# Kernel tuning notes

Measured on AMD Instinct MI355X. Metric: run time of the kernel, lower is better.

The kernel has to match this reference:

```python
import jax, jax.numpy as jnp
import numpy as np

N, CIN, T, HF, WF = 1, 64, 8, 96, 96
C = 256
H, W = HF // 4, WF // 4
K = 27  # 3 dilations (1,3,5) x 3x3 kernel taps

# kernel-tap offsets, ordered: dilation-major, then row-major 3x3 (matches cat order)
_OFFS = np.array([(oy * d, ox * d) for d in (1, 3, 5) for oy in (-1, 0, 1) for ox in (-1, 0, 1)], dtype=np.float32)


def setup_inputs() -> dict:
    key = jax.random.key(0)
    ks = jax.random.split(key, 6)
    return {
        "input": jax.random.normal(ks[0], (N, CIN, T, HF, WF), jnp.float32),
        "flow": 2.0 * jax.random.normal(ks[1], (N, 2, T, H, W), jnp.float32),
        "w_node": 0.02 * jax.random.normal(ks[2], (C, CIN, 4, 4), jnp.float32),  # Conv3d(64,256,(1,4,4)) with unit time-kernel squeezed
        "b_node": jnp.zeros((C,), jnp.float32),
        "w_up": 0.02 * jax.random.normal(ks[3], (C, 64, 4, 4), jnp.float32),  # ConvTranspose3d(256,64,(1,4,4)) weight [in,out,kh,kw]
        "b_up": jnp.zeros((64,), jnp.float32),
        "w_out": 0.05 * jax.random.normal(ks[4], (64, 64), jnp.float32),  # 1x1x1 Conv3d(64,64)
        "b_out": jnp.zeros((64,), jnp.float32),
        "B": T,
    }


def _deform_sample(node, flow):
    # Deformable neighbor sampling for all 3 dilations at once.
    # node [N,C,T,H,W], flow [N,2,T,H,W] (y,x offsets) -> neighbour [N,C,T,H,W,K]
    n, c, t, h, w = node.shape
    off = jnp.asarray(_OFFS)  # [K,2]
    yy = jnp.arange(h, dtype=node.dtype)[:, None]   # [H,1]
    xx = jnp.arange(w, dtype=node.dtype)[None, :]   # [1,W]
    # sampling positions [N,T,K,H,W]
    py = (yy + off[:, 0][:, None, None]) + flow[:, 0][:, :, None]
    px = (xx + off[:, 1][:, None, None]) + flow[:, 1][:, :, None]
    y0 = jnp.floor(py)
    x0 = jnp.floor(px)
    ty = py - y0
    tx = px - x0
    y0 = y0.astype(jnp.int32)
    x0 = x0.astype(jnp.int32)
    nf = node.transpose(0, 2, 1, 3, 4).reshape(n, t, c, h * w)  # [N,T,C,HW]

    def gather(yi, xi):
        valid = ((yi >= 0) & (yi < h) & (xi >= 0) & (xi < w)).astype(node.dtype)
        idx = jnp.clip(yi, 0, h - 1) * w + jnp.clip(xi, 0, w - 1)  # [N,T,K,H,W]
        idx = jnp.broadcast_to(idx.reshape(n, t, 1, K * h * w), (n, t, c, K * h * w))
        v = jnp.take_along_axis(nf, idx, axis=-1).reshape(n, t, c, K, h, w)
        return v * valid[:, :, None]  # zero-pad outside

    samp = (gather(y0, x0) * ((1 - ty) * (1 - tx))[:, :, None]
            + gather(y0, x0 + 1) * ((1 - ty) * tx)[:, :, None]
            + gather(y0 + 1, x0) * (ty * (1 - tx))[:, :, None]
            + gather(y0 + 1, x0 + 1) * (ty * tx)[:, :, None])  # [N,T,C,K,H,W]
    return samp.transpose(0, 2, 1, 4, 5, 3)  # [N,C,T,H,W,K]


def reference(input, flow, w_node, b_node, w_up, b_up, w_out, b_out, B):
    n, cin, t, hf, wf = input.shape
    h, w = hf // 4, wf // 4
    # layer_node: kernel==stride (1,4,4) conv == non-overlapping 4x4 patch projection
    xr = input.reshape(n, cin, t, h, 4, w, 4)
    node = jnp.einsum('ncthawb,ocab->nothw', xr, w_node) + b_node[None, :, None, None, None]  # [N,C,T,H,W]
    c = node.shape[1]

    neighbour = _deform_sample(node, flow)  # [N,C,T,H,W,27] == cat(dcn1,dcn2,dcn3)

    nhw = n * h * w
    node_b = node.transpose(0, 3, 4, 2, 1).reshape(nhw, t, c)                      # [NHW,B,C]
    nb_a = neighbour.transpose(0, 3, 4, 1, 2, 5).reshape(nhw, c, t * K)            # [NHW,C,B*27]
    A = node_b @ nb_a                                                              # [NHW,B,B*27]
    nb_b = neighbour.transpose(0, 3, 4, 2, 5, 1).reshape(nhw, t * K, c)            # [NHW,B*27,C]
    out = (1.0 / 216.0) * (A @ nb_b)                                               # [NHW,B,C]
    out = out.reshape(n, h, w, t, c).transpose(0, 4, 3, 1, 2)                      # [N,C,T,H,W]

    # layer_out: ConvTranspose (k==stride, pad 0) == per-pixel 4x4 block expansion, then 1x1x1 conv
    up = jnp.einsum('ncthw,coab->nothawb', out, w_up).reshape(n, 64, t, 4 * h, 4 * w)
    up = up + b_up[None, :, None, None, None]
    return jnp.einsum('ncthw,oc->nothw', up, w_out) + b_out[None, :, None, None, None]
```

## Files before the change

### kernel.cpp

```cpp
#include <hip/hip_runtime.h>


typedef unsigned short ushort_t;
typedef ushort_t ushort8 __attribute__((ext_vector_type(8)));
typedef __bf16 bf16x8 __attribute__((ext_vector_type(8)));
typedef __bf16 bf16x2 __attribute__((ext_vector_type(2)));
typedef float f32x4 __attribute__((ext_vector_type(4)));
typedef unsigned int uint4v __attribute__((ext_vector_type(4)));

#define NSTR 264
#define TSTR 34
#define ASTR 40

#define OFF_NH0   0
#define OFF_NH1   16896
#define OFF_NT0   33792
#define OFF_NT1   51200
#define OFF_AS    68608
#define OFF_BASES 69888
#define OFF_WTS   73472
#define ATTN_LDS  77056

__device__ __forceinline__ ushort_t f2bf(float f) {
    __bf16 h = (__bf16)f;
    return __builtin_bit_cast(ushort_t, h);
}
__device__ __forceinline__ float blo(unsigned u) { return __uint_as_float(u << 16); }
__device__ __forceinline__ float bhi(unsigned u) { return __uint_as_float(u & 0xffff0000u); }
__device__ __forceinline__ unsigned pk2(float a, float b) {
    bf16x2 v = { (__bf16)a, (__bf16)b };
    return __builtin_bit_cast(unsigned, v);
}
__device__ __forceinline__ unsigned pk2h(__bf16 a, __bf16 b) {
    bf16x2 v = { a, b };
    return __builtin_bit_cast(unsigned, v);
}
__device__ __forceinline__ void gld_lds16(const void* g, void* l) {
    __builtin_amdgcn_global_load_lds(
        (const __attribute__((address_space(1))) unsigned*)g,
        (__attribute__((address_space(3))) unsigned*)l, 16, 0, 0);
}

__global__ __launch_bounds__(256) void k_prep(
    const float* __restrict__ w_node, const float* __restrict__ w_up,
    const float* __restrict__ w_out, const float* __restrict__ b_up,
    const float* __restrict__ b_out,
    ushort_t* __restrict__ w_node_perm, ushort_t* __restrict__ Wf_perm,
    float* __restrict__ bias_tot)
{
    __shared__ float wout_s[4096];
    int tid = threadIdx.x;
    for (int i = tid; i < 4096; i += 256) wout_s[i] = w_out[i];
    __syncthreads();
    int gid = blockIdx.x * 256 + tid;
    #pragma unroll
    for (int r = 0; r < 4; ++r) {
        int e = gid + r * 65536;
        {
            int k = e & 1023, n = e >> 10;
            w_node_perm[(((k >> 3) << 8) + n) * 8 + (k & 7)] = f2bf(w_node[n * 1024 + k]);
        }
        {
            int n = e & 1023, k = e >> 10;
            int o = n >> 4, ab = n & 15;
            const float* wo = wout_s + o * 64;
            const float* wu = w_up + (k << 10) + ab;
            float s = 0.f;
            #pragma unroll 8
            for (int c = 0; c < 64; ++c) s += wo[c] * wu[c << 4];
            Wf_perm[(((k >> 3) << 10) + n) * 8 + (k & 7)] = f2bf(s);
        }
    }
    if (blockIdx.x == 0 && tid < 64) {
        float s = b_out[tid];
        const float* wo = wout_s + tid * 64;
        #pragma unroll 8
        for (int c = 0; c < 64; ++c) s += wo[c] * b_up[c];
        bias_tot[tid] = s;
    }
}

template<int FINAL>
__global__ __launch_bounds__(256) void k_gemm(
    const float* __restrict__ input, const ushort_t* __restrict__ a_bf,
    const ushort_t* __restrict__ w_perm, const float* __restrict__ bias,
    ushort_t* __restrict__ node_bf, float* __restrict__ dout)
{
    constexpr int KS = FINAL ? 4 : 16;
    constexpr int N  = FINAL ? 1024 : 256;
    constexpr int BN = FINAL ? 128 : 64;
    constexpr int NI = FINAL ? 2 : 1;
    constexpr int RB = BN / 32;
    __shared__ __align__(16) ushort_t A_lds[2][2048];
    __shared__ __align__(16) ushort_t B_lds[2][BN * 64];
    int tid  = threadIdx.x;
    int lane = tid & 63, wid = tid >> 6;
    int g = lane >> 4, r16 = lane & 15;
    int m0 = blockIdx.x * 32, n0 = blockIdx.y * BN;

    const float*   inpA = nullptr;
    const ushort_t* finA = nullptr;
    int ldsA_slot;
    if constexpr (!FINAL) {
        int mA = tid & 31, kcA = tid >> 5;
        int m = m0 + mA;
        int t = m / 576, hw = m % 576, hh = hw / 24, ww = hw % 24;
        inpA = input + (size_t)(kcA >> 1) * 73728 + t * 9216 + hh * 384 + ww * 4 + (kcA & 1) * 192;
        ldsA_slot = (kcA * 32 + mA) * 8;
    } else {
        int m = m0 + (tid >> 3), q = tid & 7;
        finA = a_bf + m * 256 + ((q ^ (m & 7)) * 8);
        ldsA_slot = tid * 8;
    }

    f32x4 acc[2][NI];
    #pragma unroll
    for (int i = 0; i < 2; ++i)
        #pragma unroll
        for (int j = 0; j < NI; ++j) acc[i][j] = (f32x4){0.f, 0.f, 0.f, 0.f};

    float4 fa, fb;
    #pragma unroll
    for (int r = 0; r < RB; ++r) {
        int s = r * 256 + tid;
        int kc = s / BN, n = s % BN;
        gld_lds16(w_perm + (size_t)((kc * N + n0 + n) * 8), &B_lds[0][s * 8]);
    }
    if constexpr (FINAL) {
        gld_lds16(finA, &A_lds[0][ldsA_slot]);
    } else {
        fa = *(const float4*)(inpA);
        fb = *(const float4*)(inpA + 96);
        uint4v p;
        p.x = pk2(fa.x, fa.y); p.y = pk2(fa.z, fa.w);
        p.z = pk2(fb.x, fb.y); p.w = pk2(fb.z, fb.w);
        *(uint4v*)&A_lds[0][ldsA_slot] = p;
    }
    __syncthreads();

    for (int kb = 0; kb < KS; ++kb) {
        int cur = kb & 1, nxt = cur ^ 1;
        bool more = (kb + 1 < KS);
        if (more) {
            #pragma unroll
            for (int r = 0; r < RB; ++r) {
                int s = r * 256 + tid;
                int kc = s / BN, n = s % BN;
                gld_lds16(w_perm + (size_t)((((kb + 1) * 8 + kc) * N + n0 + n) * 8),
                          &B_lds[nxt][s * 8]);
            }
            if constexpr (FINAL) {
                gld_lds16(finA + (kb + 1) * 64, &A_lds[nxt][ldsA_slot]);
            } else {
                fa = *(const float4*)(inpA + (size_t)(kb + 1) * 294912);
                fb = *(const float4*)(inpA + (size_t)(kb + 1) * 294912 + 96);
            }
        }
        bf16x8 af[2][2], bfr[NI][2];
        #pragma unroll
        for (int mi = 0; mi < 2; ++mi)
            #pragma unroll
            for (int ks = 0; ks < 2; ++ks) {
                int idx;
                if constexpr (!FINAL) idx = ((ks * 4 + g) * 32 + mi * 16 + r16) * 8;
                else                  idx = (mi * 16 + r16) * 64 + (((ks * 4 + g) ^ (r16 & 7)) * 8);
                af[mi][ks] = __builtin_bit_cast(bf16x8, *(const ushort8*)&A_lds[cur][idx]);
            }
        #pragma unroll
        for (int ni = 0; ni < NI; ++ni)
            #pragma unroll
            for (int ks = 0; ks < 2; ++ks) {
                int idx = ((ks * 4 + g) * BN + wid * (BN / 4) + ni * 16 + r16) * 8;
                bfr[ni][ks] = __builtin_bit_cast(bf16x8, *(const ushort8*)&B_lds[cur][idx]);
            }
        #pragma unroll
        for (int mi = 0; mi < 2; ++mi)
            #pragma unroll
            for (int ni = 0; ni < NI; ++ni)
                #pragma unroll
                for (int ks = 0; ks < 2; ++ks)
                    acc[mi][ni] = __builtin_amdgcn_mfma_f32_16x16x32_bf16(
                        af[mi][ks], bfr[ni][ks], acc[mi][ni], 0, 0, 0);
        if constexpr (!FINAL) {
            if (more) {
                uint4v p;
                p.x = pk2(fa.x, fa.y); p.y = pk2(fa.z, fa.w);
                p.z = pk2(fb.x, fb.y); p.w = pk2(fb.z, fb.w);
                *(uint4v*)&A_lds[nxt][ldsA_slot] = p;
            }
        }
        __syncthreads();
    }

    if constexpr (!FINAL) {
        int n = n0 + wid * 16 + r16;
        float bv = bias[n];
        #pragma unroll
        for (int mi = 0; mi < 2; ++mi)
            #pragma unroll
            for (int rr = 0; rr < 4; ++rr) {
                int m = m0 + mi * 16 + 4 * g + rr;
                node_bf[(size_t)m * 256 + n] = f2bf(acc[mi][0][rr] + bv);
            }
    } else {
        #pragma unroll
        for (int ni = 0; ni < NI; ++ni) {
            int n = n0 + wid * 32 + ni * 16 + r16;
            int o = n >> 4, aa = (n >> 2) & 3, bb = n & 3;
            float bv = bias[o];
            #pragma unroll
            for (int mi = 0; mi < 2; ++mi)
                #pragma unroll
                for (int rr = 0; rr < 4; ++rr) {
                    int m = m0 + mi * 16 + 4 * g + rr;
                    int t = m / 576, hw = m % 576, hh = hw / 24, ww = hw % 24;
                    dout[((size_t)(o * 8 + t) * 96 + hh * 4 + aa) * 96 + ww * 4 + bb]
                        = acc[mi][ni][rr] + bv;
                }
        }
    }
}

__device__ __forceinline__ void combine8(
    uint4v t0, uint4v t1, uint4v t2, uint4v t3,
    uint4v t4, uint4v t5, uint4v t6, uint4v t7,
    float4 wA, float4 wB, ushort_t* __restrict__ nh, ushort_t* __restrict__ nt,
    int jl, int c0)
{
    uint4v outA, outB;
    #pragma unroll
    for (int p = 0; p < 4; ++p) {
        unsigned a0 = t0[p], a1 = t1[p], a2 = t2[p], a3 = t3[p];
        unsigned b0 = t4[p], b1 = t5[p], b2 = t6[p], b3 = t7[p];
        float aL = wA.x * blo(a0) + wA.y * blo(a1) + wA.z * blo(a2) + wA.w * blo(a3);
        float aH = wA.x * bhi(a0) + wA.y * bhi(a1) + wA.z * bhi(a2) + wA.w * bhi(a3);
        float bL = wB.x * blo(b0) + wB.y * blo(b1) + wB.z * blo(b2) + wB.w * blo(b3);
        float bH = wB.x * bhi(b0) + wB.y * bhi(b1) + wB.z * bhi(b2) + wB.w * bhi(b3);
        __bf16 cAL = (__bf16)aL, cAH = (__bf16)aH;
        __bf16 cBL = (__bf16)bL, cBH = (__bf16)bH;
        outA[p] = pk2h(cAL, cAH);
        outB[p] = pk2h(cBL, cBH);
        *(unsigned*)(nt + (c0 + 2 * p) * TSTR + jl)     = pk2h(cAL, cBL);
        *(unsigned*)(nt + (c0 + 2 * p + 1) * TSTR + jl) = pk2h(cAH, cBH);
    }
    *(uint4v*)(nh + jl * NSTR + c0)       = outA;
    *(uint4v*)(nh + (jl + 1) * NSTR + c0) = outB;
}

__global__ __launch_bounds__(256) void k_attn(
    const ushort_t* __restrict__ node_bf, const float* __restrict__ flow,
    ushort_t* __restrict__ out_bf)
{
    extern __shared__ char smem[];
    ushort_t* A_s   = (ushort_t*)(smem + OFF_AS);
    int*      bases = (int*)(smem + OFF_BASES);
    float*    wts   = (float*)(smem + OFF_WTS);

    int tid  = threadIdx.x;
    int pos  = blockIdx.x;
    int h    = pos / 24, w = pos % 24;
    int lane = tid & 63, wid = tid >> 6;
    int g    = lane >> 4, r16 = lane & 15;

    if (tid < 224) {
        int j = tid;
        float w00 = 0, w01 = 0, w10 = 0, w11 = 0;
        int b00 = 0, b01 = 0, b10 = 0, b11 = 0;
        if (j < 216) {
            int tt = j / 27, kk = j - tt * 27;
            int d  = 2 * (kk / 9) + 1;
            int oy = (kk / 3) % 3 - 1, ox = kk % 3 - 1;
            float fy = flow[tt * 576 + pos];
            float fx = flow[4608 + tt * 576 + pos];
            float py = (float)(h + oy * d) + fy;
            float px = (float)(w + ox * d) + fx;
            float fy0 = floorf(py), fx0 = floorf(px);
            int y0 = (int)fy0, x0 = (int)fx0;
            float ty = py - fy0, tx = px - fx0;
            int y0c = min(max(y0, 0), 23), y1c = min(max(y0 + 1, 0), 23);
            int x0c = min(max(x0, 0), 23), x1c = min(max(x0 + 1, 0), 23);
            float vy0 = (y0 >= 0 && y0 < 24) ? 1.f : 0.f;
            float vy1 = (y0 >= -1 && y0 < 23) ? 1.f : 0.f;
            float vx0 = (x0 >= 0 && x0 < 24) ? 1.f : 0.f;
            float vx1 = (x0 >= -1 && x0 < 23) ? 1.f : 0.f;
            w00 = (1.f - ty) * (1.f - tx) * vy0 * vx0;
            w01 = (1.f - ty) * tx * vy0 * vx1;
            w10 = ty * (1.f - tx) * vy1 * vx0;
            w11 = ty * tx * vy1 * vx1;
            int base_t = tt * 576 * 256;
            b00 = base_t + (y0c * 24 + x0c) * 256;
            b01 = base_t + (y0c * 24 + x1c) * 256;
            b10 = base_t + (y1c * 24 + x0c) * 256;
            b11 = base_t + (y1c * 24 + x1c) * 256;
        }
        bases[j * 4 + 0] = b00; bases[j * 4 + 1] = b01;
        bases[j * 4 + 2] = b10; bases[j * 4 + 3] = b11;
        wts[j * 4 + 0] = w00; wts[j * 4 + 1] = w01;
        wts[j * 4 + 2] = w10; wts[j * 4 + 3] = w11;
    }
    for (int i = tid; i < 320; i += 256) ((unsigned*)A_s)[i] = 0;

    bf16x8 nbf[8];
    if (wid < 2) {
        int t = r16;
        const ushort_t* src = node_bf + ((size_t)(t & 7) * 576 + pos) * 256 + g * 8;
        ushort8 uz = {};
        #pragma unroll
        for (int s = 0; s < 8; ++s) {
            ushort8 uu = *(const ushort8*)(src + s * 32);
            nbf[s] = __builtin_bit_cast(bf16x8, (t < 8) ? uu : uz);
        }
    }

    f32x4 oacc[4];
    #pragma unroll
    for (int i = 0; i < 4; ++i) oacc[i] = (f32x4){0.f, 0.f, 0.f, 0.f};

    __syncthreads();

    const int jp2  = (tid >> 4) * 2;
    const int c0lo = (tid & 15) * 16;
    const int c0hi = c0lo + 8;

    uint4v rA0, rA1, rA2, rA3, rA4, rA5, rA6, rA7;
    uint4v rB0, rB1, rB2, rB3, rB4, rB5, rB6, rB7;

    #define PREFETCH(TILE) do {                                   \
        int jA_ = (TILE) * 32 + jp2;                              \
        int4 bsA_ = *(const int4*)&bases[jA_ * 4];                \
        int4 bsB_ = *(const int4*)&bases[jA_ * 4 + 4];            \
        rA0 = *(const uint4v*)(node_bf + bsA_.x + c0lo);          \
        rA1 = *(const uint4v*)(node_bf + bsA_.y + c0lo);          \
        rA2 = *(const uint4v*)(node_bf + bsA_.z + c0lo);          \
        rA3 = *(const uint4v*)(node_bf + bsA_.w + c0lo);          \
        rA4 = *(const uint4v*)(node_bf + bsB_.x + c0lo);          \
        rA5 = *(const uint4v*)(node_bf + bsB_.y + c0lo);          \
        rA6 = *(const uint4v*)(node_bf + bsB_.z + c0lo);          \
        rA7 = *(const uint4v*)(node_bf + bsB_.w + c0lo);          \
        rB0 = *(const uint4v*)(node_bf + bsA_.x + c0hi);          \
        rB1 = *(const uint4v*)(node_bf + bsA_.y + c0hi);          \
        rB2 = *(const uint4v*)(node_bf + bsA_.z + c0hi);          \
        rB3 = *(const uint4v*)(node_bf + bsA_.w + c0hi);          \
        rB4 = *(const uint4v*)(node_bf + bsB_.x + c0hi);          \
        rB5 = *(const uint4v*)(node_bf + bsB_.y + c0hi);          \
        rB6 = *(const uint4v*)(node_bf + bsB_.z + c0hi);          \
        rB7 = *(const uint4v*)(node_bf + bsB_.w + c0hi);          \
    } while (0)

    #define COMBINE(TILE, nh, nt) do {                                          \
        int jC_ = (TILE) * 32 + jp2;                                            \
        float4 wA_ = *(const float4*)&wts[jC_ * 4];                             \
        float4 wB_ = *(const float4*)&wts[jC_ * 4 + 4];                         \
        combine8(rA0, rA1, rA2, rA3, rA4, rA5, rA6, rA7, wA_, wB_, nh, nt, jp2, c0lo); \
        combine8(rB0, rB1, rB2, rB3, rB4, rB5, rB6, rB7, wA_, wB_, nh, nt, jp2, c0hi); \
    } while (0)

    PREFETCH(0);
    COMBINE(0, (ushort_t*)(smem + OFF_NH0), (ushort_t*)(smem + OFF_NT0));
    PREFETCH(1);
    __syncthreads();

    for (int k = 0; k < 7; ++k) {
        int cur = k & 1;
        ushort_t* nh = (ushort_t*)(smem + (cur ? OFF_NH1 : OFF_NH0));
        ushort_t* nt = (ushort_t*)(smem + (cur ? OFF_NT1 : OFF_NT0));

        if (wid < 2) {
            f32x4 aacc = {0.f, 0.f, 0.f, 0.f};
            int jbase = wid * 16;
            #pragma unroll
            for (int s = 0; s < 8; ++s) {
                const ushort_t* bp = nh + (jbase + r16) * NSTR + s * 32 + g * 8;
                bf16x8 bfrag = __builtin_bit_cast(bf16x8, *(const ushort8*)bp);
                aacc = __builtin_amdgcn_mfma_f32_16x16x32_bf16(nbf[s], bfrag, aacc, 0, 0, 0);
            }
            if (g < 2) {
                #pragma unroll
                for (int rr = 0; rr < 4; ++rr)
                    A_s[(4 * g + rr) * ASTR + jbase + r16] = f2bf(aacc[rr] * (1.f / 216.f));
            }
        }
        __syncthreads();

        {
            bf16x8 afrag = __builtin_bit_cast(bf16x8, *(const ushort8*)(A_s + r16 * ASTR + g * 8));
            #pragma unroll
            for (int i = 0; i < 4; ++i) {
                const ushort_t* tp = nt + (wid * 64 + i * 16 + r16) * TSTR + g * 8;
                uint4v uv;
                uv.x = *(const unsigned*)(tp);
                uv.y = *(const unsigned*)(tp + 2);
                uv.z = *(const unsigned*)(tp + 4);
                uv.w = *(const unsigned*)(tp + 6);
                bf16x8 bfrag = __builtin_bit_cast(bf16x8, uv);
                oacc[i] = __builtin_amdgcn_mfma_f32_16x16x32_bf16(afrag, bfrag, oacc[i], 0, 0, 0);
            }
        }
        if (k < 6) {
            ushort_t* nh2 = (ushort_t*)(smem + (cur ? OFF_NH0 : OFF_NH1));
            ushort_t* nt2 = (ushort_t*)(smem + (cur ? OFF_NT0 : OFF_NT1));
            COMBINE(k + 1, nh2, nt2);
            if (k <= 4) PREFETCH(k + 2);
        }
        __syncthreads();
    }
    #undef PREFETCH
    #undef COMBINE

    if (g < 2) {
        #pragma unroll
        for (int i = 0; i < 4; ++i) {
            int c = wid * 64 + i * 16 + r16;
            #pragma unroll
            for (int rr = 0; rr < 4; ++rr) {
                int t = 4 * g + rr;
                out_bf[((size_t)t * 576 + pos) * 256 + c] = f2bf(oacc[i][rr]);
            }
        }
    }
}

extern "C" void kernel_launch(void* const* d_in, const int* in_sizes, int n_in,
                              void* d_out, int out_size, void* d_ws, size_t ws_size,
                              hipStream_t stream) {
    (void)in_sizes; (void)n_in; (void)out_size; (void)ws_size;
    const float* input  = (const float*)d_in[0];
    const float* flow   = (const float*)d_in[1];
    const float* w_node = (const float*)d_in[2];
    const float* b_node = (const float*)d_in[3];
    const float* w_up   = (const float*)d_in[4];
    const float* b_up   = (const float*)d_in[5];
    const float* w_out  = (const float*)d_in[6];
    const float* b_out  = (const float*)d_in[7];
    float* dout = (float*)d_out;

    char* wsb = (char*)d_ws;
    ushort_t* node_bf = (ushort_t*)wsb;
    ushort_t* out_bf  = (ushort_t*)(wsb + 2359296);
    ushort_t* w_np    = (ushort_t*)(wsb + 4718592);
    ushort_t* wf_p    = (ushort_t*)(wsb + 5242880);
    float*    bias_t  = (float*)(wsb + 5767168);

    k_prep<<<256, 256, 0, stream>>>(w_node, w_up, w_out, b_up, b_out, w_np, wf_p, bias_t);
    k_gemm<0><<<dim3(144, 4), 256, 0, stream>>>(input, nullptr, w_np, b_node, node_bf, nullptr);
    hipFuncSetAttribute(reinterpret_cast<const void*>(k_attn),
                        hipFuncAttributeMaxDynamicSharedMemorySize, ATTN_LDS);
    k_attn<<<576, 256, ATTN_LDS, stream>>>(node_bf, flow, out_bf);
    k_gemm<1><<<dim3(144, 8), 256, 0, stream>>>(nullptr, out_bf, wf_p, bias_t, nullptr, dout);
}
```

Baseline: 74.62 us.

## Drop transposed neighbour LDS copy, stage final GEMM epilogue through LDS

The attention kernel no longer writes a second, transposed copy of the sampled neighbour tile into LDS. The second MFMA now builds its B fragments with eight strided 16-bit LDS reads from the row-major tile, which roughly halves LDS use per block and may allow more blocks per CU, at the cost of more LDS read instructions. The final GEMM epilogue now stages accumulators in LDS so each thread can write a float4 to the output instead of scattered scalar stores. The weight-prep reduction also gets four independent accumulators to shorten its dependency chain.

```diff
diff --git a/kernel.cpp b/kernel.cpp
--- a/kernel.cpp
+++ b/kernel.cpp
@@ -9,17 +9,14 @@
 typedef unsigned int uint4v __attribute__((ext_vector_type(4)));
 
 #define NSTR 264
-#define TSTR 34
 #define ASTR 40
 
 #define OFF_NH0   0
 #define OFF_NH1   16896
-#define OFF_NT0   33792
-#define OFF_NT1   51200
-#define OFF_AS    68608
-#define OFF_BASES 69888
-#define OFF_WTS   73472
-#define ATTN_LDS  77056
+#define OFF_AS    33792
+#define OFF_BASES 35072
+#define OFF_WTS   38656
+#define ATTN_LDS  42240
 
 __device__ __forceinline__ ushort_t f2bf(float f) {
     __bf16 h = (__bf16)f;
@@ -29,10 +26,6 @@
 __device__ __forceinline__ float bhi(unsigned u) { return __uint_as_float(u & 0xffff0000u); }
 __device__ __forceinline__ unsigned pk2(float a, float b) {
     bf16x2 v = { (__bf16)a, (__bf16)b };
-    return __builtin_bit_cast(unsigned, v);
-}
-__device__ __forceinline__ unsigned pk2h(__bf16 a, __bf16 b) {
-    bf16x2 v = { a, b };
     return __builtin_bit_cast(unsigned, v);
 }
 __device__ __forceinline__ void gld_lds16(const void* g, void* l) {
@@ -65,10 +58,15 @@
             int o = n >> 4, ab = n & 15;
             const float* wo = wout_s + o * 64;
             const float* wu = w_up + (k << 10) + ab;
-            float s = 0.f;
-            #pragma unroll 8
-            for (int c = 0; c < 64; ++c) s += wo[c] * wu[c << 4];
-            Wf_perm[(((k >> 3) << 10) + n) * 8 + (k & 7)] = f2bf(s);
+            float s0 = 0.f, s1 = 0.f, s2 = 0.f, s3 = 0.f;
+            #pragma unroll 4
+            for (int c = 0; c < 64; c += 4) {
+                s0 += wo[c]     * wu[c << 4];
+                s1 += wo[c + 1] * wu[(c + 1) << 4];
+                s2 += wo[c + 2] * wu[(c + 2) << 4];
+                s3 += wo[c + 3] * wu[(c + 3) << 4];
+            }
+            Wf_perm[(((k >> 3) << 10) + n) * 8 + (k & 7)] = f2bf((s0 + s1) + (s2 + s3));
         }
     }
     if (blockIdx.x == 0 && tid < 64) {
@@ -203,20 +201,30 @@
                 node_bf[(size_t)m * 256 + n] = f2bf(acc[mi][0][rr] + bv);
             }
     } else {
+        constexpr int EPS = 132;
+        float* ep = (float*)&B_lds[0][0];
         #pragma unroll
         for (int ni = 0; ni < NI; ++ni) {
-            int n = n0 + wid * 32 + ni * 16 + r16;
-            int o = n >> 4, aa = (n >> 2) & 3, bb = n & 3;
-            float bv = bias[o];
+            int n = wid * 32 + ni * 16 + r16;
             #pragma unroll
             for (int mi = 0; mi < 2; ++mi)
                 #pragma unroll
-                for (int rr = 0; rr < 4; ++rr) {
-                    int m = m0 + mi * 16 + 4 * g + rr;
-                    int t = m / 576, hw = m % 576, hh = hw / 24, ww = hw % 24;
-                    dout[((size_t)(o * 8 + t) * 96 + hh * 4 + aa) * 96 + ww * 4 + bb]
-                        = acc[mi][ni][rr] + bv;
-                }
+                for (int rr = 0; rr < 4; ++rr)
+                    ep[(mi * 16 + 4 * g + rr) * EPS + n] = acc[mi][ni][rr];
+        }
+        __syncthreads();
+        #pragma unroll
+        for (int r = 0; r < 4; ++r) {
+            int task = r * 256 + tid;
+            int mloc = task & 31, nb4 = task >> 5;
+            float4 v = *(const float4*)&ep[mloc * EPS + nb4 * 4];
+            int n = n0 + nb4 * 4;
+            int o = n >> 4, aa = (n >> 2) & 3;
+            float bv = bias[o];
+            int m = m0 + mloc;
+            int t = m / 576, hw = m % 576, hh = hw / 24, ww = hw % 24;
+            float* dst = dout + ((size_t)(o * 8 + t) * 96 + hh * 4 + aa) * 96 + ww * 4;
+            *(float4*)dst = make_float4(v.x + bv, v.y + bv, v.z + bv, v.w + bv);
         }
     }
 }
@@ -224,8 +232,7 @@
 __device__ __forceinline__ void combine8(
     uint4v t0, uint4v t1, uint4v t2, uint4v t3,
     uint4v t4, uint4v t5, uint4v t6, uint4v t7,
-    float4 wA, float4 wB, ushort_t* __restrict__ nh, ushort_t* __restrict__ nt,
-    int jl, int c0)
+    float4 wA, float4 wB, ushort_t* __restrict__ nh, int jl, int c0)
 {
     uint4v outA, outB;
     #pragma unroll
@@ -236,12 +243,8 @@
         float aH = wA.x * bhi(a0) + wA.y * bhi(a1) + wA.z * bhi(a2) + wA.w * bhi(a3);
         float bL = wB.x * blo(b0) + wB.y * blo(b1) + wB.z * blo(b2) + wB.w * blo(b3);
         float bH = wB.x * bhi(b0) + wB.y * bhi(b1) + wB.z * bhi(b2) + wB.w * bhi(b3);
-        __bf16 cAL = (__bf16)aL, cAH = (__bf16)aH;
-        __bf16 cBL = (__bf16)bL, cBH = (__bf16)bH;
-        outA[p] = pk2h(cAL, cAH);
-        outB[p] = pk2h(cBL, cBH);
-        *(unsigned*)(nt + (c0 + 2 * p) * TSTR + jl)     = pk2h(cAL, cBL);
-        *(unsigned*)(nt + (c0 + 2 * p + 1) * TSTR + jl) = pk2h(cAH, cBH);
+        outA[p] = pk2(aL, aH);
+        outB[p] = pk2(bL, bH);
     }
     *(uint4v*)(nh + jl * NSTR + c0)       = outA;
     *(uint4v*)(nh + (jl + 1) * NSTR + c0) = outB;
@@ -347,23 +350,22 @@
         rB7 = *(const uint4v*)(node_bf + bsB_.w + c0hi);          \
     } while (0)
 
-    #define COMBINE(TILE, nh, nt) do {                                          \
+    #define COMBINE(TILE, nh) do {                                              \
         int jC_ = (TILE) * 32 + jp2;                                            \
         float4 wA_ = *(const float4*)&wts[jC_ * 4];                             \
         float4 wB_ = *(const float4*)&wts[jC_ * 4 + 4];                         \
-        combine8(rA0, rA1, rA2, rA3, rA4, rA5, rA6, rA7, wA_, wB_, nh, nt, jp2, c0lo); \
-        combine8(rB0, rB1, rB2, rB3, rB4, rB5, rB6, rB7, wA_, wB_, nh, nt, jp2, c0hi); \
+        combine8(rA0, rA1, rA2, rA3, rA4, rA5, rA6, rA7, wA_, wB_, nh, jp2, c0lo); \
+        combine8(rB0, rB1, rB2, rB3, rB4, rB5, rB6, rB7, wA_, wB_, nh, jp2, c0hi); \
     } while (0)
 
     PREFETCH(0);
-    COMBINE(0, (ushort_t*)(smem + OFF_NH0), (ushort_t*)(smem + OFF_NT0));
+    COMBINE(0, (ushort_t*)(smem + OFF_NH0));
     PREFETCH(1);
     __syncthreads();
 
     for (int k = 0; k < 7; ++k) {
         int cur = k & 1;
         ushort_t* nh = (ushort_t*)(smem + (cur ? OFF_NH1 : OFF_NH0));
-        ushort_t* nt = (ushort_t*)(smem + (cur ? OFF_NT1 : OFF_NT0));
 
         if (wid < 2) {
             f32x4 aacc = {0.f, 0.f, 0.f, 0.f};
@@ -386,20 +388,17 @@
             bf16x8 afrag = __builtin_bit_cast(bf16x8, *(const ushort8*)(A_s + r16 * ASTR + g * 8));
             #pragma unroll
             for (int i = 0; i < 4; ++i) {
-                const ushort_t* tp = nt + (wid * 64 + i * 16 + r16) * TSTR + g * 8;
-                uint4v uv;
-                uv.x = *(const unsigned*)(tp);
-                uv.y = *(const unsigned*)(tp + 2);
-                uv.z = *(const unsigned*)(tp + 4);
-                uv.w = *(const unsigned*)(tp + 6);
-                bf16x8 bfrag = __builtin_bit_cast(bf16x8, uv);
+                int cc = wid * 64 + i * 16 + r16;
+                ushort8 bv;
+                #pragma unroll
+                for (int e = 0; e < 8; ++e) bv[e] = nh[(g * 8 + e) * NSTR + cc];
+                bf16x8 bfrag = __builtin_bit_cast(bf16x8, bv);
                 oacc[i] = __builtin_amdgcn_mfma_f32_16x16x32_bf16(afrag, bfrag, oacc[i], 0, 0, 0);
             }
         }
         if (k < 6) {
             ushort_t* nh2 = (ushort_t*)(smem + (cur ? OFF_NH0 : OFF_NH1));
-            ushort_t* nt2 = (ushort_t*)(smem + (cur ? OFF_NT0 : OFF_NT1));
-            COMBINE(k + 1, nh2, nt2);
+            COMBINE(k + 1, nh2);
             if (k <= 4) PREFETCH(k + 2);
         }
         __syncthreads();
```

Measured after the change: 64.59 us. 1.16x faster.
